# Kernel tuning notes

Hardware: AMD Instinct MI355X
Metric: run time of the kernel (lower is better)

The kernel has to match this reference:

```python
import jax, jax.numpy as jnp
import numpy as np

NQ = 8            # data qubits: ceil(log2(256))
NLAYERS = 6       # StronglyEntanglingLayers depth
BATCH = 4096
IN_DIM = 2560
ENC_DIM = 256

def leaky(x):
    return jnp.where(x >= 0, x, 0.2 * x)

def rot_mat(phi, theta, omega):
    # PennyLane Rot(phi,theta,omega) = RZ(omega) @ RY(theta) @ RZ(phi)
    c = jnp.cos(theta / 2); s = jnp.sin(theta / 2)
    m00 = jnp.exp(-0.5j * (phi + omega)) * c
    m01 = -jnp.exp(0.5j * (phi - omega)) * s
    m10 = jnp.exp(-0.5j * (phi - omega)) * s
    m11 = jnp.exp(0.5j * (phi + omega)) * c
    return jnp.stack([jnp.stack([m00, m01]), jnp.stack([m10, m11])])

def apply_1q(psi, U, w):
    psi = jnp.tensordot(U, psi, axes=((1,), (w,)))
    return jnp.moveaxis(psi, 0, w)

def apply_cnot(psi, c, t):
    s = jnp.moveaxis(psi, (c, t), (0, 1))
    s = jnp.stack([s[0], s[1, ::-1]], axis=0)
    return jnp.moveaxis(s, (0, 1), (c, t))

def circuit(amps, params):
    # amps: (256,) complex64 normalized amplitudes; params: (L, NQ, 3)
    psi = amps.reshape((2,) * NQ)
    L = params.shape[0]
    for l in range(L):
        for q in range(NQ):
            psi = apply_1q(psi, rot_mat(params[l, q, 0], params[l, q, 1], params[l, q, 2]), q)
        r = l % (NQ - 1) + 1  # PennyLane default imprimitive ranges
        for q in range(NQ):
            psi = apply_cnot(psi, q, (q + r) % NQ)
    probs = jnp.real(psi * jnp.conj(psi))
    z, xm, ym = [], [], []
    yfac_base = jnp.array([-1j, 1j], dtype=psi.dtype)
    for q in range(NQ):
        axes = tuple(i for i in range(NQ) if i != q)
        p = jnp.sum(probs, axis=axes)
        z.append(p[0] - p[1])
        flipped = jnp.flip(psi, axis=q)
        xm.append(jnp.real(jnp.sum(jnp.conj(psi) * flipped)))
        yfac = yfac_base.reshape([2 if i == q else 1 for i in range(NQ)])
        ym.append(jnp.real(jnp.sum(jnp.conj(psi) * (flipped * yfac))))
    return jnp.stack(z + xm + ym)  # (24,) order: Z..., X..., Y...

def forward(x, ew1, eb1, ew2, eb2, ew3, eb3, dec_params,
            dw1, db1, dw2, db2, dw3, db3, dw4, db4, dw5, db5):
    h = leaky(x @ ew1 + eb1)
    h = leaky(h @ ew2 + eb2)
    enc = jnp.tanh(h @ ew3 + eb3)                      # (B, 256)
    nrm = jnp.linalg.norm(enc, axis=1, keepdims=True)
    amps = jax.lax.stop_gradient(enc / jnp.maximum(nrm, 1e-12)).astype(jnp.complex64)
    meas = jax.vmap(lambda a: circuit(a, dec_params))(amps)  # (B, 24)
    h = leaky(meas @ dw1 + db1)
    h = leaky(h @ dw2 + db2)
    h = leaky(h @ dw3 + db3)
    h = leaky(h @ dw4 + db4)
    return jnp.tanh(h @ dw5 + db5)                     # (B, 2560)

def _lin(key, fin, fout):
    k1, k2 = jax.random.split(key)
    lim = 1.0 / np.sqrt(fin)
    w = jax.random.uniform(k1, (fin, fout), jnp.float32, -lim, lim)
    b = jax.random.uniform(k2, (fout,), jnp.float32, -lim, lim)
    return w, b

def setup_inputs() -> dict:
    key = jax.random.key(0)
    ks = jax.random.split(key, 10)
    x = jax.random.normal(ks[0], (BATCH, IN_DIM), jnp.float32)
    ew1, eb1 = _lin(ks[1], IN_DIM, 1024)
    ew2, eb2 = _lin(ks[2], 1024, 512)
    ew3, eb3 = _lin(ks[3], 512, ENC_DIM)
    dec_params = jax.random.uniform(ks[4], (NLAYERS, NQ, 3), jnp.float32, 0.0, 2 * np.pi)
    dw1, db1 = _lin(ks[5], 3 * NQ, 128)
    dw2, db2 = _lin(ks[6], 128, 256)
    dw3, db3 = _lin(ks[7], 256, 512)
    dw4, db4 = _lin(ks[8], 512, 1024)
    dw5, db5 = _lin(ks[9], 1024, IN_DIM)
    return {"x": x, "ew1": ew1, "eb1": eb1, "ew2": ew2, "eb2": eb2, "ew3": ew3, "eb3": eb3,
            "dec_params": dec_params, "dw1": dw1, "db1": db1, "dw2": dw2, "db2": db2,
            "dw3": dw3, "db3": db3, "dw4": dw4, "db4": db4, "dw5": dw5, "db5": db5}

def reference(x, ew1, eb1, ew2, eb2, ew3, eb3, dec_params,
              dw1, db1, dw2, db2, dw3, db3, dw4, db4, dw5, db5):
    return forward(x, ew1, eb1, ew2, eb2, ew3, eb3, dec_params,
                   dw1, db1, dw2, db2, dw3, db3, dw4, db4, dw5, db5)
```

## Files before the change

### kernel.cpp

```cpp
#include <hip/hip_runtime.h>
#include <hip/hip_bf16.h>


using bf16 = __hip_bfloat16;
typedef __attribute__((ext_vector_type(8))) short short8;
typedef __attribute__((ext_vector_type(4))) short short4v;
typedef __attribute__((ext_vector_type(4))) float f32x4;

__device__ inline void stf(float* p, size_t i, float v) { p[i] = v; }
__device__ inline void stf(bf16* p, size_t i, float v) { p[i] = __float2bfloat16(v); }

__device__ inline float fast_tanh(float x) {
  x = fminf(fmaxf(x, -15.0f), 15.0f);
  float t = __expf(2.0f * x);
  return __fdividef(t - 1.0f, t + 1.0f);
}

__device__ inline short f2bs(float x) {
  bf16 h = __float2bfloat16(x);
  return *reinterpret_cast<short*>(&h);
}
__device__ inline short8 ld8b(const float* p) {
  const float4 a = ((const float4*)p)[0];
  const float4 b = ((const float4*)p)[1];
  short8 r;
  r[0] = f2bs(a.x); r[1] = f2bs(a.y); r[2] = f2bs(a.z); r[3] = f2bs(a.w);
  r[4] = f2bs(b.x); r[5] = f2bs(b.y); r[6] = f2bs(b.z); r[7] = f2bs(b.w);
  return r;
}
__device__ inline short4v ld4b(const float* p) {
  const float4 a = *(const float4*)p;
  short4v r;
  r[0] = f2bs(a.x); r[1] = f2bs(a.y); r[2] = f2bs(a.z); r[3] = f2bs(a.w);
  return r;
}

__device__ inline void async_load16(const bf16* g, short* l) {
  __builtin_amdgcn_global_load_lds(
      (const __attribute__((address_space(1))) unsigned int*)g,
      (__attribute__((address_space(3))) unsigned int*)l, 16, 0, 0);
}

__device__ inline void run_circuit(float (&re)[4], float (&im)[4],
                                   const float* gsh, int lane) {
  for (int l = 0; l < 6; ++l) {
    for (int qq = 0; qq < 8; ++qq) {
      const float* g = &gsh[(l * 8 + qq) * 8];
      const int s = 1 << (7 - qq);
      if (s >= 4) {
        const int lm = s >> 2;
        const bool hi = (lane & lm) != 0;
        const float g0r = hi ? g[4] : g[0], g0i = hi ? g[5] : g[1];
        const float g1r = hi ? g[6] : g[2], g1i = hi ? g[7] : g[3];
#pragma unroll
        for (int j = 0; j < 4; ++j) {
          float orr = __shfl_xor(re[j], lm, 64);
          float oii = __shfl_xor(im[j], lm, 64);
          float p0r = hi ? orr : re[j], p0i = hi ? oii : im[j];
          float p1r = hi ? re[j] : orr, p1i = hi ? im[j] : oii;
          re[j] = g0r * p0r - g0i * p0i + g1r * p1r - g1i * p1i;
          im[j] = g0r * p0i + g0i * p0r + g1r * p1i + g1i * p1r;
        }
      } else {
#pragma unroll
        for (int j0 = 0; j0 < 4; ++j0) {
          if ((j0 & s) == 0) {
            int j1 = j0 | s;
            float p0r = re[j0], p0i = im[j0], p1r = re[j1], p1i = im[j1];
            re[j0] = g[0] * p0r - g[1] * p0i + g[2] * p1r - g[3] * p1i;
            im[j0] = g[0] * p0i + g[1] * p0r + g[2] * p1i + g[3] * p1r;
            re[j1] = g[4] * p0r - g[5] * p0i + g[6] * p1r - g[7] * p1i;
            im[j1] = g[4] * p0i + g[5] * p0r + g[6] * p1i + g[7] * p1r;
          }
        }
      }
    }
    const int r = l % 7 + 1;
    for (int qq = 0; qq < 8; ++qq) {
      const int sc = 1 << (7 - qq);
      const int st = 1 << (7 - ((qq + r) & 7));
      if (st >= 4) {
        const int lm = st >> 2;
        if (sc >= 4) {
          const bool ctl = (lane & (sc >> 2)) != 0;
#pragma unroll
          for (int j = 0; j < 4; ++j) {
            float orr = __shfl_xor(re[j], lm, 64);
            float oii = __shfl_xor(im[j], lm, 64);
            re[j] = ctl ? orr : re[j];
            im[j] = ctl ? oii : im[j];
          }
        } else {
#pragma unroll
          for (int j = 0; j < 4; ++j) {
            if (j & sc) {
              re[j] = __shfl_xor(re[j], lm, 64);
              im[j] = __shfl_xor(im[j], lm, 64);
            }
          }
        }
      } else {
        if (sc >= 4) {
          const bool ctl = (lane & (sc >> 2)) != 0;
#pragma unroll
          for (int j0 = 0; j0 < 4; ++j0) {
            if ((j0 & st) == 0) {
              int j1 = j0 | st;
              float t0r = re[j0], t0i = im[j0];
              float t1r = re[j1], t1i = im[j1];
              re[j0] = ctl ? t1r : t0r; im[j0] = ctl ? t1i : t0i;
              re[j1] = ctl ? t0r : t1r; im[j1] = ctl ? t0i : t1i;
            }
          }
        } else {
#pragma unroll
          for (int j0 = 0; j0 < 4; ++j0) {
            if ((j0 & sc) && (j0 & st) == 0) {
              int j1 = j0 | st;
              float tr = re[j0], ti = im[j0];
              re[j0] = re[j1]; im[j0] = im[j1];
              re[j1] = tr; im[j1] = ti;
            }
          }
        }
      }
    }
  }
}

__global__ __launch_bounds__(256) void prep_all(
    const float* w0, const float* w1, const float* w2, const float* w3,
    const float* w4, const float* w5, const float* w6, const float* w7,
    const float* b0, const float* b1, const float* b2, const float* b3,
    const float* b4, const float* b5, const float* b6, const float* b7,
    const float* dp, const float* xf,
    bf16* __restrict__ wt, float* __restrict__ biasf, float* __restrict__ gw,
    bf16* __restrict__ xb, bf16* __restrict__ btu, int do_x) {
  int bid = blockIdx.x;
  const int tid = threadIdx.x;

  if (bid < 64) {
    __shared__ float gsh[384];
    if (tid < 48) {
      float phi = dp[tid * 3 + 0], theta = dp[tid * 3 + 1], omega = dp[tid * 3 + 2];
      float c = cosf(0.5f * theta), s = sinf(0.5f * theta);
      float a = 0.5f * (phi + omega), d = 0.5f * (phi - omega);
      float ca = cosf(a), sa = sinf(a), cd = cosf(d), sd = sinf(d);
      float* o = &gsh[tid * 8];
      o[0] =  ca * c; o[1] = -sa * c;
      o[2] = -cd * s; o[3] = -sd * s;
      o[4] =  cd * s; o[5] = -sd * s;
      o[6] =  ca * c; o[7] =  sa * c;
    }
    __syncthreads();
    const int lane = tid & 63;
    const int col = bid * 4 + (tid >> 6);
    float re[4], im[4];
#pragma unroll
    for (int j = 0; j < 4; ++j) { re[j] = (lane * 4 + j == col) ? 1.f : 0.f; im[j] = 0.f; }
    run_circuit(re, im, gsh, lane);
#pragma unroll
    for (int j = 0; j < 4; ++j) {
      int n = lane * 4 + j;
      {
        bf16 h = __float2bfloat16(re[j]);
        float lo = re[j] - __bfloat162float(h);
        size_t base = (size_t)n * 768 + col;
        btu[base] = h; btu[base + 256] = h; btu[base + 512] = __float2bfloat16(lo);
      }
      {
        bf16 h = __float2bfloat16(im[j]);
        float lo = im[j] - __bfloat162float(h);
        size_t base = (size_t)(256 + n) * 768 + col;
        btu[base] = h; btu[base + 256] = h; btu[base + 512] = __float2bfloat16(lo);
      }
    }
    return;
  }
  bid -= 64;

  const int Ks[8]  = {2560, 1024, 512, 24, 128, 256, 512, 1024};
  const int Ns[8]  = {1024, 512, 256, 128, 256, 512, 1024, 2560};
  const int cum[8] = {2560, 3072, 3200, 3204, 3236, 3364, 3876, 6436};
  const long wto[8] = {0, 2621440, 3145728, 3276800, 3280896, 3313664, 3444736, 3969024};
  const float* Wp[8] = {w0, w1, w2, w3, w4, w5, w6, w7};
  const float* Bp[8] = {b0, b1, b2, b3, b4, b5, b6, b7};
  const int boff[8] = {0, 1024, 1536, 1792, 1920, 2176, 2688, 3712};

  if (bid < 6436) {
    int t = 0;
    while (bid >= cum[t]) t++;
    int base = t ? cum[t - 1] : 0;
    int local = bid - base;
    int K = Ks[t], N = Ns[t];
    int tk = (K + 31) >> 5;
    int kt = local % tk, nt = local / tk;
    int Kp = tk << 5;
    __shared__ short tile[32][33];
    int r = tid >> 3, c4 = (tid & 7) << 2;
    int gk = kt * 32 + r, gn = nt * 32 + c4;
    short4v v;
    if (gk < K) v = ld4b(Wp[t] + (size_t)gk * N + gn);
    else { v[0] = 0; v[1] = 0; v[2] = 0; v[3] = 0; }
    tile[r][c4] = v[0]; tile[r][c4 + 1] = v[1]; tile[r][c4 + 2] = v[2]; tile[r][c4 + 3] = v[3];
    __syncthreads();
    int n = tid >> 3, k4 = (tid & 7) << 2;
    short4v o;
    o[0] = tile[k4][n]; o[1] = tile[k4 + 1][n]; o[2] = tile[k4 + 2][n]; o[3] = tile[k4 + 3][n];
    *(short4v*)&wt[wto[t] + (size_t)(nt * 32 + n) * Kp + kt * 32 + k4] = o;
  } else if (bid < 6444) {
    int b = bid - 6436;
    int nb = Ns[b];
    for (int t2 = tid; t2 < nb; t2 += 256)
      biasf[boff[b] + t2] = Bp[b][t2];
  } else if (bid == 6444) {
    int g = tid;
    if (g < 48) {
      float phi = dp[g * 3 + 0], theta = dp[g * 3 + 1], omega = dp[g * 3 + 2];
      float c = cosf(0.5f * theta), s = sinf(0.5f * theta);
      float a = 0.5f * (phi + omega), d = 0.5f * (phi - omega);
      float ca = cosf(a), sa = sinf(a), cd = cosf(d), sd = sinf(d);
      float* o = gw + g * 8;
      o[0] =  ca * c; o[1] = -sa * c;
      o[2] = -cd * s; o[3] = -sd * s;
      o[4] =  cd * s; o[5] = -sd * s;
      o[6] =  ca * c; o[7] =  sa * c;
    }
  } else if (do_x) {
    long i = ((long)(bid - 6445) * 256 + tid) * 8;
    if (i < 10485760L) {
      short8 v = ld8b(xf + i);
      *(short8*)((short*)xb + i) = v;
    }
  }
}

template <int BM, int BN, int BK, int WR, int WC, int ACT, typename TC>
__global__ __launch_bounds__(256) void gemm_async(const bf16* __restrict__ A,
                                                  const bf16* __restrict__ Bt,
                                                  const float* __restrict__ bias,
                                                  TC* __restrict__ C,
                                                  int M, int N, int K) {
  constexpr int CPR = BK / 8;
  constexpr int MASK = CPR - 1;
  constexpr int RPW = 64 / CPR;
  constexpr int RPP = 4 * RPW;
  constexpr int WMT = BM / WR;
  constexpr int WNT = BN / WC;
  constexpr int FI = WMT / 16;
  constexpr int FJ = WNT / 16;
  constexpr int KK = BK / 32;
  __shared__ __align__(16) short As[2][BM * BK];
  __shared__ __align__(16) short Bs[2][BN * BK];
  const int tid = threadIdx.x;
  const int lane = tid & 63;
  const int wid = tid >> 6;
  const int wm = wid / WC, wn = wid % WC;
  const int bm = blockIdx.y * BM;
  const int bn = blockIdx.x * BN;

  const int st_r = lane / CPR;
  const int st_cs = (lane & MASK) ^ (st_r & MASK);

  const int frag_m = lane & 15;
  const int q = lane >> 4;

  auto stage = [&](int buf, int k0) {
#pragma unroll
    for (int p = 0; p < BM / RPP; ++p) {
      const bf16* g = A + (size_t)(bm + p * RPP + wid * RPW + st_r) * K + k0 + st_cs * 8;
      async_load16(g, &As[buf][(p * RPP + wid * RPW) * BK]);
    }
#pragma unroll
    for (int p = 0; p < BN / RPP; ++p) {
      const bf16* g = Bt + (size_t)(bn + p * RPP + wid * RPW + st_r) * K + k0 + st_cs * 8;
      async_load16(g, &Bs[buf][(p * RPP + wid * RPW) * BK]);
    }
  };

  f32x4 acc[FI][FJ] = {};

  stage(0, 0);
  __syncthreads();

  const int nsteps = K / BK;
  int cur = 0;
  for (int t = 0; t < nsteps; ++t) {
    if (t + 1 < nsteps) stage(cur ^ 1, (t + 1) * BK);

    short8 af[FI][KK], bfr[FJ][KK];
#pragma unroll
    for (int i = 0; i < FI; ++i) {
      const int m = wm * WMT + i * 16 + frag_m;
#pragma unroll
      for (int kk = 0; kk < KK; ++kk) {
        const int slot = (kk * 4 + q) ^ (m & MASK);
        af[i][kk] = *(const short8*)&As[cur][m * BK + slot * 8];
      }
    }
#pragma unroll
    for (int j = 0; j < FJ; ++j) {
      const int n = wn * WNT + j * 16 + frag_m;
#pragma unroll
      for (int kk = 0; kk < KK; ++kk) {
        const int slot = (kk * 4 + q) ^ (n & MASK);
        bfr[j][kk] = *(const short8*)&Bs[cur][n * BK + slot * 8];
      }
    }
#pragma unroll
    for (int kk = 0; kk < KK; ++kk)
#pragma unroll
      for (int i = 0; i < FI; ++i)
#pragma unroll
        for (int j = 0; j < FJ; ++j)
          acc[i][j] = __builtin_amdgcn_mfma_f32_16x16x32_bf16(af[i][kk], bfr[j][kk], acc[i][j], 0, 0, 0);

    __syncthreads();
    cur ^= 1;
  }

  const int col_lane = lane & 15;
  const int row_quad = q << 2;
#pragma unroll
  for (int i = 0; i < FI; ++i) {
#pragma unroll
    for (int j = 0; j < FJ; ++j) {
      int n = bn + wn * WNT + j * 16 + col_lane;
      float bj = (ACT == 2) ? 0.f : bias[n];
#pragma unroll
      for (int r = 0; r < 4; ++r) {
        int m = bm + wm * WMT + i * 16 + row_quad + r;
        float v = acc[i][j][r] + bj;
        if (ACT == 0) {
          v = (v >= 0.f) ? v : 0.2f * v;
          stf(C, (size_t)m * N + n, v);
        } else if (ACT == 1) {
          stf(C, (size_t)m * N + n, fast_tanh(v));
        } else if (ACT == 2) {
          stf(C, (size_t)m * N + n, v);
        } else {
          float tv = fast_tanh(v);
          bf16 h = __float2bfloat16(tv);
          float lo = tv - __bfloat162float(h);
          size_t base = (size_t)m * 768 + n;
          ((bf16*)C)[base] = h;
          ((bf16*)C)[base + 256] = __float2bfloat16(lo);
          ((bf16*)C)[base + 512] = h;
        }
      }
    }
  }
}

__global__ __launch_bounds__(256) void gemm_cvt(const float* __restrict__ A,
                                                const float* __restrict__ W,
                                                const float* __restrict__ bias,
                                                bf16* __restrict__ C,
                                                int M, int N, int K) {
  __shared__ __align__(16) short As[128 * 40];
  __shared__ __align__(16) short Bs[128 * 40];
  const int tid = threadIdx.x;
  const int lane = tid & 63;
  const int wave = tid >> 6;
  const int wm = wave >> 1, wn = wave & 1;
  const int bm = blockIdx.y * 128;
  const int bn = blockIdx.x * 128;
  const int a_row0 = tid >> 2;
  const int a_kcol = (tid & 3) << 3;
  const int b_ncol = (tid & 31) << 2;
  const int b_krow = (tid >> 5) << 2;
  const int frag_m = lane & 15;
  const int frag_k = (lane >> 4) << 3;

  f32x4 acc[4][4] = {};

  for (int k0 = 0; k0 < K; k0 += 32) {
#pragma unroll
    for (int c = 0; c < 2; ++c) {
      const int row = c * 64 + a_row0;
      short8 v = ld8b(A + (size_t)(bm + row) * K + k0 + a_kcol);
      *(short8*)&As[row * 40 + a_kcol] = v;
    }
    short4v bv[4];
#pragma unroll
    for (int kk = 0; kk < 4; ++kk)
      bv[kk] = ld4b(W + (size_t)(k0 + b_krow + kk) * N + bn + b_ncol);
#pragma unroll
    for (int nn = 0; nn < 4; ++nn) {
      short4v w;
      w[0] = bv[0][nn]; w[1] = bv[1][nn]; w[2] = bv[2][nn]; w[3] = bv[3][nn];
      *(short4v*)&Bs[(b_ncol + nn) * 40 + b_krow] = w;
    }
    __syncthreads();
    short8 af[4], bfr[4];
#pragma unroll
    for (int i = 0; i < 4; ++i)
      af[i] = *(const short8*)&As[(wm * 64 + i * 16 + frag_m) * 40 + frag_k];
#pragma unroll
    for (int j = 0; j < 4; ++j)
      bfr[j] = *(const short8*)&Bs[(wn * 64 + j * 16 + frag_m) * 40 + frag_k];
#pragma unroll
    for (int i = 0; i < 4; ++i)
#pragma unroll
      for (int j = 0; j < 4; ++j)
        acc[i][j] = __builtin_amdgcn_mfma_f32_16x16x32_bf16(af[i], bfr[j], acc[i][j], 0, 0, 0);
    __syncthreads();
  }

  const int col_lane = lane & 15;
  const int row_quad = (lane >> 4) << 2;
#pragma unroll
  for (int i = 0; i < 4; ++i)
#pragma unroll
    for (int j = 0; j < 4; ++j) {
      int n = bn + wn * 64 + j * 16 + col_lane;
      float bj = bias[n];
#pragma unroll
      for (int r = 0; r < 4; ++r) {
        int m = bm + wm * 64 + i * 16 + row_quad + r;
        float v = acc[i][j][r] + bj;
        v = (v >= 0.f) ? v : 0.2f * v;
        stf(C, (size_t)m * N + n, v);
      }
    }
}

__global__ __launch_bounds__(256) void meas_d1(const float* __restrict__ PSI,
                                               const float* __restrict__ dw1,
                                               const float* __restrict__ db1,
                                               bf16* __restrict__ d1out) {
  const int tid = threadIdx.x;
  const int lane = tid & 63;
  const int b = blockIdx.x * 4 + (tid >> 6);

  const float* pp = PSI + (size_t)b * 512;
  float4 ar = *(const float4*)(pp + lane * 4);
  float4 ai = *(const float4*)(pp + 256 + lane * 4);
  float re[4] = {ar.x, ar.y, ar.z, ar.w};
  float im[4] = {ai.x, ai.y, ai.z, ai.w};

  float ss = 0.f;
#pragma unroll
  for (int j = 0; j < 4; ++j) ss += re[j] * re[j] + im[j] * im[j];
#pragma unroll
  for (int o = 32; o; o >>= 1) ss += __shfl_xor(ss, o, 64);
  const float inv = 1.0f / fmaxf(ss, 1e-24f);

  float mz[8], mx[8], my[8];
#pragma unroll
  for (int qq = 0; qq < 8; ++qq) {
    const int s = 1 << (7 - qq);
    float z = 0.f, x = 0.f, y = 0.f;
#pragma unroll
    for (int j = 0; j < 4; ++j) {
      float fr, fi;
      if (s >= 4) {
        fr = __shfl_xor(re[j], s >> 2, 64);
        fi = __shfl_xor(im[j], s >> 2, 64);
      } else {
        fr = re[j ^ s]; fi = im[j ^ s];
      }
      float prob = re[j] * re[j] + im[j] * im[j];
      int i = lane * 4 + j;
      float sg = (i & s) ? -1.f : 1.f;
      z += sg * prob;
      x += re[j] * fr + im[j] * fi;
      y += sg * (re[j] * fi - im[j] * fr);
    }
#pragma unroll
    for (int o = 32; o; o >>= 1) {
      z += __shfl_xor(z, o, 64);
      x += __shfl_xor(x, o, 64);
      y += __shfl_xor(y, o, 64);
    }
    mz[qq] = z * inv; mx[qq] = x * inv; my[qq] = y * inv;
  }

#pragma unroll
  for (int half = 0; half < 2; ++half) {
    const int n = lane + half * 64;
    float acc = db1[n];
#pragma unroll
    for (int qq = 0; qq < 8; ++qq) {
      acc += mz[qq] * dw1[qq * 128 + n];
      acc += mx[qq] * dw1[(8 + qq) * 128 + n];
      acc += my[qq] * dw1[(16 + qq) * 128 + n];
    }
    acc = (acc >= 0.f) ? acc : 0.2f * acc;
    d1out[(size_t)b * 128 + n] = __float2bfloat16(acc);
  }
}

__global__ __launch_bounds__(256) void circuit_wave(const float* __restrict__ enc,
                                                    const float* __restrict__ gw,
                                                    const float* __restrict__ dw1,
                                                    const float* __restrict__ db1,
                                                    bf16* __restrict__ d1out) {
  __shared__ float gsh[384];
  const int tid = threadIdx.x;
  for (int t = tid; t < 384; t += 256) gsh[t] = gw[t];
  __syncthreads();
  const int lane = tid & 63;
  const int b = blockIdx.x * 4 + (tid >> 6);

  float4 e = *(const float4*)(enc + (size_t)b * 256 + lane * 4);
  float re[4] = {e.x, e.y, e.z, e.w};
  float im[4] = {0.f, 0.f, 0.f, 0.f};
  float ss = e.x * e.x + e.y * e.y + e.z * e.z + e.w * e.w;
#pragma unroll
  for (int o = 32; o; o >>= 1) ss += __shfl_xor(ss, o, 64);
  float inv = 1.0f / fmaxf(sqrtf(ss), 1e-12f);
#pragma unroll
  for (int j = 0; j < 4; ++j) re[j] *= inv;

  run_circuit(re, im, gsh, lane);

  float mz[8], mx[8], my[8];
#pragma unroll
  for (int qq = 0; qq < 8; ++qq) {
    const int s = 1 << (7 - qq);
    float z = 0.f, x = 0.f, y = 0.f;
#pragma unroll
    for (int j = 0; j < 4; ++j) {
      float fr, fi;
      if (s >= 4) {
        fr = __shfl_xor(re[j], s >> 2, 64);
        fi = __shfl_xor(im[j], s >> 2, 64);
      } else {
        fr = re[j ^ s]; fi = im[j ^ s];
      }
      float prob = re[j] * re[j] + im[j] * im[j];
      int i = lane * 4 + j;
      float sg = (i & s) ? -1.f : 1.f;
      z += sg * prob;
      x += re[j] * fr + im[j] * fi;
      y += sg * (re[j] * fi - im[j] * fr);
    }
#pragma unroll
    for (int o = 32; o; o >>= 1) {
      z += __shfl_xor(z, o, 64);
      x += __shfl_xor(x, o, 64);
      y += __shfl_xor(y, o, 64);
    }
    mz[qq] = z; mx[qq] = x; my[qq] = y;
  }

#pragma unroll
  for (int half = 0; half < 2; ++half) {
    const int n = lane + half * 64;
    float acc = db1[n];
#pragma unroll
    for (int qq = 0; qq < 8; ++qq) {
      acc += mz[qq] * dw1[qq * 128 + n];
      acc += mx[qq] * dw1[(8 + qq) * 128 + n];
      acc += my[qq] * dw1[(16 + qq) * 128 + n];
    }
    acc = (acc >= 0.f) ? acc : 0.2f * acc;
    d1out[(size_t)b * 128 + n] = __float2bfloat16(acc);
  }
}

extern "C" void kernel_launch(void* const* d_in, const int* in_sizes, int n_in,
                              void* d_out, int out_size, void* d_ws, size_t ws_size,
                              hipStream_t stream) {
  (void)in_sizes; (void)n_in; (void)out_size;
  char* wsb = (char*)d_ws;
  float* gw    = (float*)(wsb + 256);
  float* biasf = (float*)(wsb + 4096);
  float* encf  = (float*)(wsb + 294912);
  bf16*  BtU   = (bf16*)(wsb + 294912);
  bf16*  P     = (bf16*)(wsb + 4489216);
  bf16*  Q     = (bf16*)(wsb + 12877824);
  bf16*  WT    = (bf16*)(wsb + 17072128);
  bf16*  Xb    = (bf16*)(wsb + 30253056);
  bf16*  Ap    = (bf16*)(wsb + 30253056);
  float* PSI   = (float*)(wsb + 36544512);
  const bool have_xb = ws_size >= 51224576;

  bf16* ew1t = WT + 0;
  bf16* ew2t = WT + 2621440;
  bf16* ew3t = WT + 3145728;
  bf16* dw2t = WT + 3280896;
  bf16* dw3t = WT + 3313664;
  bf16* dw4t = WT + 3444736;
  bf16* dw5t = WT + 3969024;
  float* beb1 = biasf + 0;
  float* beb2 = biasf + 1024;
  float* beb3 = biasf + 1536;
  float* bdb2 = biasf + 1920;
  float* bdb3 = biasf + 2176;
  float* bdb4 = biasf + 2688;
  float* bdb5 = biasf + 3712;

  prep_all<<<11629, 256, 0, stream>>>(
      (const float*)d_in[1], (const float*)d_in[3], (const float*)d_in[5],
      (const float*)d_in[8], (const float*)d_in[10], (const float*)d_in[12],
      (const float*)d_in[14], (const float*)d_in[16],
      (const float*)d_in[2], (const float*)d_in[4], (const float*)d_in[6],
      (const float*)d_in[9], (const float*)d_in[11], (const float*)d_in[13],
      (const float*)d_in[15], (const float*)d_in[17],
      (const float*)d_in[7], (const float*)d_in[0],
      WT, biasf, gw, Xb, BtU, have_xb ? 1 : 0);

  if (have_xb) {
    gemm_async<128, 64, 64, 4, 1, 0, bf16><<<dim3(16, 32), 256, 0, stream>>>(
        Xb, ew1t, beb1, P, 4096, 1024, 2560);
  } else {
    gemm_cvt<<<dim3(8, 32), 256, 0, stream>>>(
        (const float*)d_in[0], (const float*)d_in[1], beb1, P, 4096, 1024, 2560);
  }

  gemm_async<64, 64, 64, 2, 2, 0, bf16><<<dim3(8, 64), 256, 0, stream>>>(
      P, ew2t, beb2, Q, 4096, 512, 1024);

  if (have_xb) {
    gemm_async<64, 64, 64, 2, 2, 3, bf16><<<dim3(4, 64), 256, 0, stream>>>(
        Q, ew3t, beb3, Ap, 4096, 256, 512);
    gemm_async<64, 64, 64, 2, 2, 2, float><<<dim3(8, 64), 256, 0, stream>>>(
        Ap, BtU, beb3 , PSI, 4096, 512, 768);
    meas_d1<<<1024, 256, 0, stream>>>(PSI, (const float*)d_in[8],
                                      (const float*)d_in[9], Q);
  } else {
    gemm_async<64, 64, 64, 2, 2, 1, float><<<dim3(4, 64), 256, 0, stream>>>(
        Q, ew3t, beb3, encf, 4096, 256, 512);
    circuit_wave<<<1024, 256, 0, stream>>>(encf, gw, (const float*)d_in[8],
                                           (const float*)d_in[9], Q);
  }

  gemm_async<64, 64, 64, 2, 2, 0, bf16><<<dim3(4, 64), 256, 0, stream>>>(
      Q, dw2t, bdb2, P, 4096, 256, 128);
  gemm_async<64, 64, 64, 2, 2, 0, bf16><<<dim3(8, 64), 256, 0, stream>>>(
      P, dw3t, bdb3, Q, 4096, 512, 256);
  gemm_async<128, 64, 64, 4, 1, 0, bf16><<<dim3(16, 32), 256, 0, stream>>>(
      Q, dw4t, bdb4, P, 4096, 1024, 512);
  gemm_async<128, 128, 64, 2, 2, 1, float><<<dim3(20, 32), 256, 0, stream>>>(
      P, dw5t, bdb5, (float*)d_out, 4096, 2560, 1024);
}
```

Before: 299.0 us.

## Restructure async GEMM pipeline to prefetch two stages ahead with explicit vmcnt waits

The async-load GEMM now issues loads for the first two K tiles up front. Each iteration waits with a partial vmcnt so only the current tile must have arrived. The next-next tile load is issued after the fragments are read into registers and a barrier, which lets it overlap the MFMA work, and the last tile is peeled out of the loop. This replaces the single __syncthreads-per-step double buffer, in exchange for hand-written waitcnt literals that assume a fixed number of outstanding loads per stage.

```diff
diff --git a/kernel.cpp b/kernel.cpp
--- a/kernel.cpp
+++ b/kernel.cpp
@@ -250,6 +250,8 @@
   constexpr int FI = WMT / 16;
   constexpr int FJ = WNT / 16;
   constexpr int KK = BK / 32;
+  constexpr int LOADS = BM / RPP + BN / RPP;
+  static_assert(LOADS == 4 || LOADS == 6 || LOADS == 8, "vmcnt literal");
   __shared__ __align__(16) short As[2][BM * BK];
   __shared__ __align__(16) short Bs[2][BN * BK];
   const int tid = threadIdx.x;
@@ -280,14 +282,18 @@
 
   f32x4 acc[FI][FJ] = {};
 
+  const int nsteps = K / BK;
   stage(0, 0);
-  __syncthreads();
-
-  const int nsteps = K / BK;
-  int cur = 0;
-  for (int t = 0; t < nsteps; ++t) {
-    if (t + 1 < nsteps) stage(cur ^ 1, (t + 1) * BK);
-
+  if (nsteps > 1) stage(1, BK);
+
+  for (int t = 0; t < nsteps - 1; ++t) {
+    if constexpr (LOADS == 8) asm volatile("s_waitcnt vmcnt(8)" ::: "memory");
+    else if constexpr (LOADS == 6) asm volatile("s_waitcnt vmcnt(6)" ::: "memory");
+    else asm volatile("s_waitcnt vmcnt(4)" ::: "memory");
+    __builtin_amdgcn_s_barrier();
+
+    const short* Ac = As[t & 1];
+    const short* Bc = Bs[t & 1];
     short8 af[FI][KK], bfr[FJ][KK];
 #pragma unroll
     for (int i = 0; i < FI; ++i) {
@@ -295,7 +301,7 @@
 #pragma unroll
       for (int kk = 0; kk < KK; ++kk) {
         const int slot = (kk * 4 + q) ^ (m & MASK);
-        af[i][kk] = *(const short8*)&As[cur][m * BK + slot * 8];
+        af[i][kk] = *(const short8*)&Ac[m * BK + slot * 8];
       }
     }
 #pragma unroll
@@ -304,9 +310,15 @@
 #pragma unroll
       for (int kk = 0; kk < KK; ++kk) {
         const int slot = (kk * 4 + q) ^ (n & MASK);
-        bfr[j][kk] = *(const short8*)&Bs[cur][n * BK + slot * 8];
-      }
-    }
+        bfr[j][kk] = *(const short8*)&Bs[t & 1][n * BK + slot * 8];
+      }
+    }
+    (void)Bc;
+    asm volatile("s_waitcnt lgkmcnt(0)" ::: "memory");
+    __builtin_amdgcn_sched_barrier(0);
+    __builtin_amdgcn_s_barrier();
+    if (t + 2 < nsteps) stage(t & 1, (t + 2) * BK);
+
 #pragma unroll
     for (int kk = 0; kk < KK; ++kk)
 #pragma unroll
@@ -314,9 +326,40 @@
 #pragma unroll
         for (int j = 0; j < FJ; ++j)
           acc[i][j] = __builtin_amdgcn_mfma_f32_16x16x32_bf16(af[i][kk], bfr[j][kk], acc[i][j], 0, 0, 0);
-
-    __syncthreads();
-    cur ^= 1;
+  }
+
+  asm volatile("s_waitcnt vmcnt(0)" ::: "memory");
+  __builtin_amdgcn_s_barrier();
+  {
+    const int t = nsteps - 1;
+    const short* Ac = As[t & 1];
+    const short* Bc = Bs[t & 1];
+    short8 af[FI][KK], bfr[FJ][KK];
+#pragma unroll
+    for (int i = 0; i < FI; ++i) {
+      const int m = wm * WMT + i * 16 + frag_m;
+#pragma unroll
+      for (int kk = 0; kk < KK; ++kk) {
+        const int slot = (kk * 4 + q) ^ (m & MASK);
+        af[i][kk] = *(const short8*)&Ac[m * BK + slot * 8];
+      }
+    }
+#pragma unroll
+    for (int j = 0; j < FJ; ++j) {
+      const int n = wn * WNT + j * 16 + frag_m;
+#pragma unroll
+      for (int kk = 0; kk < KK; ++kk) {
+        const int slot = (kk * 4 + q) ^ (n & MASK);
+        bfr[j][kk] = *(const short8*)&Bc[n * BK + slot * 8];
+      }
+    }
+#pragma unroll
+    for (int kk = 0; kk < KK; ++kk)
+#pragma unroll
+      for (int i = 0; i < FI; ++i)
+#pragma unroll
+        for (int j = 0; j < FJ; ++j)
+          acc[i][j] = __builtin_amdgcn_mfma_f32_16x16x32_bf16(af[i][kk], bfr[j][kk], acc[i][j], 0, 0, 0);
   }
 
   const int col_lane = lane & 15;
```

Result: faster. 276.5 us (-7.5%).
